# Kernel tuning notes

Hardware: AMD Instinct MI355X
Metric: run time of the kernel (lower is better)

The kernel has to match this reference:

```python
import jax, jax.numpy as jnp
import numpy as np

N_NODES = 100000
N_EDGES = 3200000
IN_DIM, HID_DIM, OUT_DIM = 512, 256, 64


def setup_inputs() -> dict:
    key = jax.random.key(0)
    k1, k2, k3, k4, k5, k6 = jax.random.split(key, 6)
    x = jax.random.normal(k1, (N_NODES, IN_DIM), dtype=jnp.float32)
    src = jax.random.randint(k2, (N_EDGES,), 0, N_NODES, dtype=jnp.int32)
    dst = jax.random.randint(k3, (N_EDGES,), 0, N_NODES, dtype=jnp.int32)
    edge_index = jnp.stack([src, dst])  # [2, E]: row 0 = src (column), row 1 = dst (row)
    edge_weight = jax.random.uniform(k4, (N_EDGES,), dtype=jnp.float32)
    # Xavier-uniform init like nn.init.xavier_uniform_
    lim1 = float(np.sqrt(6.0 / (IN_DIM + HID_DIM)))
    lim2 = float(np.sqrt(6.0 / (HID_DIM + OUT_DIM)))
    W1 = jax.random.uniform(k5, (IN_DIM, HID_DIM), minval=-lim1, maxval=lim1, dtype=jnp.float32)
    W2 = jax.random.uniform(k6, (HID_DIM, OUT_DIM), minval=-lim2, maxval=lim2, dtype=jnp.float32)
    return {"x": x, "edge_index": edge_index, "edge_weight": edge_weight, "W1": W1, "W2": W2}


def _spmm(edge_index, edge_weight, support):
    # out[dst] += w * support[src]  (sparse adjacency @ dense support)
    src, dst = edge_index[0], edge_index[1]
    msgs = support[src] * edge_weight[:, None]  # [E, F]
    return jax.ops.segment_sum(msgs, dst, num_segments=N_NODES)


def reference(x, edge_index, edge_weight, W1, W2):
    # Layer 1: dense GEMM then SpMM, then ReLU (dropout is identity in eval)
    h = _spmm(edge_index, edge_weight, x @ W1)
    h = jax.nn.relu(h)
    # Layer 2
    out = _spmm(edge_index, edge_weight, h @ W2)
    return jax.nn.softmax(out, axis=1)
```

## Files before the change

### kernel.cpp

```cpp
#include <hip/hip_runtime.h>
#include <hip/hip_bf16.h>

typedef __attribute__((ext_vector_type(8))) short bf16x8;
typedef __attribute__((ext_vector_type(4))) float f32x4;
typedef __attribute__((ext_vector_type(4))) _Float16 f16x4;
typedef unsigned short ushort_t;

#define NN   100000
#define NE   3200000
#define IND  512
#define HIDD 256
#define OUTD 64

#define NBKT 98
#define P1E  2048
#define MPAN 782

__device__ __forceinline__ ushort_t f2bf(float a) {
    unsigned u = __float_as_uint(a);
    unsigned r = (u + 0x7FFFu + ((u >> 16) & 1u)) >> 16;
    return (ushort_t)r;
}
__device__ __forceinline__ float bf2f(ushort_t b) {
    return __uint_as_float(((unsigned)b) << 16);
}

union U8 { ushort_t us[8]; unsigned u32[4]; uint4 v; };

#define GLOAD_LDS16(gp, lp) \
    __builtin_amdgcn_global_load_lds( \
        (const __attribute__((address_space(1))) void*)(const void*)(gp), \
        (__attribute__((address_space(3))) void*)(void*)(lp), 16, 0, 0)

__device__ __forceinline__ void split8(float4 v0, float4 v1, bf16x8& aH, bf16x8& aL) {
    float vv[8] = {v0.x, v0.y, v0.z, v0.w, v1.x, v1.y, v1.z, v1.w};
    U8 H, L;
    #pragma unroll
    for (int j = 0; j < 4; ++j) {
        unsigned u0 = __float_as_uint(vv[2 * j]);
        unsigned u1 = __float_as_uint(vv[2 * j + 1]);
        H.u32[j] = __builtin_amdgcn_perm(u1, u0, 0x07060302u);
        float r0 = vv[2 * j]     - __uint_as_float(u0 & 0xFFFF0000u);
        float r1 = vv[2 * j + 1] - __uint_as_float(u1 & 0xFFFF0000u);
        L.u32[j] = __builtin_amdgcn_perm(__float_as_uint(r1),
                                         __float_as_uint(r0), 0x07060302u);
    }
    aH = *(const bf16x8*)&H.v;
    aL = *(const bf16x8*)&L.v;
}

__global__ void splitw_k(const float* __restrict__ in, ushort_t* __restrict__ thi,
                         ushort_t* __restrict__ tlo, int R, int C) {
    int i = blockIdx.x * 256 + threadIdx.x;
    if (i < R * C) {
        int r = i / C, c = i % C;
        float a = in[i];
        ushort_t h = f2bf(a);
        thi[(size_t)c * R + r] = h;
        tlo[(size_t)c * R + r] = f2bf(a - bf2f(h));
    }
}

__global__ __launch_bounds__(256, 3) void gemm1_k(
    const float* __restrict__ A, const ushort_t* __restrict__ BtHi,
    const ushort_t* __restrict__ BtLo, _Float16* __restrict__ C)
{
    const int M = NN, N = HIDD, K = IND;
    __shared__ __align__(16) float    sA [128 * 32];
    __shared__ __align__(16) ushort_t sBh[128 * 32];
    __shared__ __align__(16) ushort_t sBl[128 * 32];

    const int bid   = blockIdx.x;
    const int grp   = bid >> 4;
    const int rr_   = bid & 15;
    const int panel = grp * 8 + (rr_ & 7);
    if (panel >= MPAN) return;
    const int m0 = panel * 128;
    const int n0 = (rr_ >> 3) * 128;

    const int tid  = threadIdx.x;
    const int wave = tid >> 6;
    const int lane = tid & 63;
    const int quad = lane >> 4;
    const int l15  = lane & 15;
    const int wr   = wave >> 1;
    const int wc   = wave & 1;

    const float* aSrc[4];
    float*       aDst[4];
    #pragma unroll
    for (int it = 0; it < 4; ++it) {
        int f = it * 256 + tid;
        int r = f >> 3;
        int bp = (f & 7) ^ ((r & 3) << 1) ^ ((r >> 2) & 1);
        int gr = m0 + r; if (gr >= M) gr = M - 1;
        aSrc[it] = A + (size_t)gr * K + bp * 4;
        aDst[it] = &sA[f * 4];
    }
    const ushort_t* bhSrc[2]; const ushort_t* blSrc[2];
    ushort_t* bhDst[2]; ushort_t* blDst[2];
    #pragma unroll
    for (int it = 0; it < 2; ++it) {
        int f = it * 256 + tid;
        int r = f >> 2;
        int qp = (f & 3) ^ ((r >> 1) & 3);
        bhSrc[it] = BtHi + (size_t)(n0 + r) * K + qp * 8;
        blSrc[it] = BtLo + (size_t)(n0 + r) * K + qp * 8;
        bhDst[it] = &sBh[f * 8];
        blDst[it] = &sBl[f * 8];
    }

    int aOff[4][2];
    #pragma unroll
    for (int ms = 0; ms < 4; ++ms) {
        int rA = wr * 64 + ms * 16 + l15;
        int sw = ((rA & 3) << 1) ^ ((rA >> 2) & 1);
        int cb = quad << 1;
        aOff[ms][0] = rA * 32 + (((cb    ) ^ sw) << 2);
        aOff[ms][1] = rA * 32 + (((cb | 1) ^ sw) << 2);
    }
    int bOff[4];
    #pragma unroll
    for (int ns = 0; ns < 4; ++ns) {
        int rB = wc * 64 + ns * 16 + l15;
        bOff[ns] = rB * 32 + (quad ^ ((rB >> 1) & 3)) * 8;
    }

    f32x4 acc[4][4] = {};

    for (int k0 = 0; k0 < K; k0 += 32) {
        #pragma unroll
        for (int it = 0; it < 4; ++it) GLOAD_LDS16(aSrc[it] + k0, aDst[it]);
        #pragma unroll
        for (int it = 0; it < 2; ++it) {
            GLOAD_LDS16(bhSrc[it] + k0, bhDst[it]);
            GLOAD_LDS16(blSrc[it] + k0, blDst[it]);
        }
        __syncthreads();

        bf16x8 aH[4], aL[4];
        #pragma unroll
        for (int ms = 0; ms < 4; ++ms) {
            float4 v0 = *(const float4*)&sA[aOff[ms][0]];
            float4 v1 = *(const float4*)&sA[aOff[ms][1]];
            split8(v0, v1, aH[ms], aL[ms]);
        }

        #pragma unroll
        for (int ns = 0; ns < 4; ++ns) {
            bf16x8 bH = *(const bf16x8*)&sBh[bOff[ns]];
            bf16x8 bL = *(const bf16x8*)&sBl[bOff[ns]];
            #pragma unroll
            for (int ms = 0; ms < 4; ++ms) {
                acc[ms][ns] = __builtin_amdgcn_mfma_f32_16x16x32_bf16(aH[ms], bH, acc[ms][ns], 0, 0, 0);
                acc[ms][ns] = __builtin_amdgcn_mfma_f32_16x16x32_bf16(aL[ms], bH, acc[ms][ns], 0, 0, 0);
                acc[ms][ns] = __builtin_amdgcn_mfma_f32_16x16x32_bf16(aH[ms], bL, acc[ms][ns], 0, 0, 0);
            }
        }
        __syncthreads();
    }

    #pragma unroll
    for (int ms = 0; ms < 4; ++ms) {
        int row = m0 + wr * 64 + ms * 16 + quad * 4;
        #pragma unroll
        for (int ns = 0; ns < 4; ++ns) {
            int col = n0 + wc * 64 + ns * 16 + l15;
            #pragma unroll
            for (int r = 0; r < 4; ++r)
                if (row + r < M) C[(size_t)(row + r) * N + col] = (_Float16)acc[ms][ns][r];
        }
    }
}

__global__ __launch_bounds__(256) void bhist_k(const int* __restrict__ dst,
                                               int* __restrict__ bucketHist) {
    __shared__ int h[NBKT];
    int t = threadIdx.x;
    if (t < NBKT) h[t] = 0;
    __syncthreads();
    #pragma unroll
    for (int j = 0; j < 4; ++j) {
        int e = blockIdx.x * 1024 + t + j * 256;
        if (e < NE) atomicAdd(&h[dst[e] >> 10], 1);
    }
    __syncthreads();
    if (t < NBKT && h[t]) atomicAdd(&bucketHist[t], h[t]);
}

__global__ __launch_bounds__(128) void bscan_k(const int* __restrict__ bucketHist,
                                               int* __restrict__ bucketStart,
                                               int* __restrict__ bucketCursor) {
    __shared__ int s[128];
    int t = threadIdx.x;
    int v = (t < NBKT) ? bucketHist[t] : 0;
    s[t] = v;
    for (int off = 1; off < 128; off <<= 1) {
        __syncthreads();
        int a = (t >= off) ? s[t - off] : 0;
        __syncthreads();
        s[t] += a;
    }
    __syncthreads();
    if (t < NBKT) { bucketStart[t] = s[t] - v; bucketCursor[t] = s[t] - v; }
    if (t == NBKT - 1) bucketStart[NBKT] = s[t];
}

__global__ __launch_bounds__(256) void phase1_k(
    const int* __restrict__ src, const int* __restrict__ dst,
    const float* __restrict__ w, int* __restrict__ bucketCursor,
    int2* __restrict__ binned)
{
    __shared__ int2 raw[P1E];
    __shared__ int2 ord[P1E];
    __shared__ ushort_t rbkt[P1E], obkt[P1E];
    __shared__ int hist[128], excl[128], cursor[128], gbase[128], stmp[128];

    int t = threadIdx.x;
    if (t < 128) hist[t] = 0;
    __syncthreads();

    int e0 = blockIdx.x * P1E;
    #pragma unroll
    for (int j = 0; j < P1E / 256; ++j) {
        int li = t + j * 256;
        int e = e0 + li;
        if (e < NE) {
            int d = dst[e];
            int b = d >> 10;
            raw[li] = make_int2(src[e] | ((d & 1023) << 17), __float_as_int(w[e]));
            rbkt[li] = (ushort_t)b;
            atomicAdd(&hist[b], 1);
        } else rbkt[li] = 0xFFFFu;
    }
    __syncthreads();
    int v = (t < 128) ? hist[t] : 0;
    if (t < 128) stmp[t] = v;
    for (int off = 1; off < 128; off <<= 1) {
        __syncthreads();
        int a = (t < 128 && t >= off) ? stmp[t - off] : 0;
        __syncthreads();
        if (t < 128) stmp[t] += a;
    }
    __syncthreads();
    if (t < 128) { excl[t] = stmp[t] - v; cursor[t] = stmp[t] - v; }
    if (t < NBKT) gbase[t] = atomicAdd(&bucketCursor[t], hist[t]);
    __syncthreads();
    #pragma unroll
    for (int j = 0; j < P1E / 256; ++j) {
        int li = t + j * 256;
        ushort_t b = rbkt[li];
        if (b != 0xFFFFu) {
            int p = atomicAdd(&cursor[b], 1);
            ord[p] = raw[li];
            obkt[p] = b;
        }
    }
    __syncthreads();
    int tot = excl[NBKT - 1] + hist[NBKT - 1];
    #pragma unroll
    for (int j = 0; j < P1E / 256; ++j) {
        int li = t + j * 256;
        if (li < tot) {
            int b = obkt[li];
            binned[(size_t)gbase[b] + (li - excl[b])] = ord[li];
        }
    }
}

__global__ __launch_bounds__(256) void phase2_k(
    const int* __restrict__ bucketStart, const int2* __restrict__ binned,
    int* __restrict__ rowptr, int2* __restrict__ esw)
{
    __shared__ int cnt[1024], ex[1024], cur[1024], wsum[256];
    int t = threadIdx.x, blk = blockIdx.x;
    int gb = bucketStart[blk], ge = bucketStart[blk + 1];
    #pragma unroll
    for (int j = 0; j < 4; ++j) cnt[t + j * 256] = 0;
    __syncthreads();
    for (int e = gb + t; e < ge; e += 256)
        atomicAdd(&cnt[(binned[e].x >> 17) & 1023], 1);
    __syncthreads();
    int b4 = t * 4;
    int l0 = cnt[b4], l1 = cnt[b4 + 1], l2 = cnt[b4 + 2], l3 = cnt[b4 + 3];
    int ls = l0 + l1 + l2 + l3;
    wsum[t] = ls;
    for (int off = 1; off < 256; off <<= 1) {
        __syncthreads();
        int a = (t >= off) ? wsum[t - off] : 0;
        __syncthreads();
        wsum[t] += a;
    }
    __syncthreads();
    int be = wsum[t] - ls;
    ex[b4] = be;            cur[b4] = be;
    ex[b4 + 1] = be + l0;     cur[b4 + 1] = be + l0;
    ex[b4 + 2] = be + l0 + l1;  cur[b4 + 2] = be + l0 + l1;
    ex[b4 + 3] = be + l0 + l1 + l2; cur[b4 + 3] = be + l0 + l1 + l2;
    __syncthreads();
    int n0 = blk << 10;
    #pragma unroll
    for (int j = 0; j < 4; ++j) {
        int i = b4 + j;
        if (n0 + i < NN) rowptr[n0 + i] = gb + ex[i];
    }
    if (blk == NBKT - 1 && t == 0) rowptr[NN] = NE;
    for (int e = gb + t; e < ge; e += 256) {
        int2 en = binned[e];
        int d = (en.x >> 17) & 1023;
        int p = atomicAdd(&cur[d], 1);
        esw[(size_t)gb + p] = make_int2(en.x & 0x1FFFF, en.y);
    }
}

__global__ __launch_bounds__(256) void spmm_relu_gemm2_k(
    const int* __restrict__ rowptr, const int2* __restrict__ esw,
    const _Float16* __restrict__ X, const ushort_t* __restrict__ BtHi,
    const ushort_t* __restrict__ BtLo, _Float16* __restrict__ S2)
{
    __shared__ __align__(16) float h[16][260];

    const int wave  = threadIdx.x >> 6;
    const int lane  = threadIdx.x & 63;
    const int quad  = lane >> 4;
    const int l15   = lane & 15;
    const int nbase = blockIdx.x * 16;

    const _Float16* Xl = X + lane * 4;
    #pragma unroll
    for (int i = 0; i < 4; ++i) {
        const int ln   = wave * 4 + i;
        const int node = nbase + ln;
        const int beg = rowptr[node], end = rowptr[node + 1];
        f32x4 acc = {0.f, 0.f, 0.f, 0.f};
        #pragma unroll 8
        for (int e = beg; e < end; ++e) {
            int2 sw = esw[e];
            float w = __int_as_float(sw.y);
            f16x4 v = *(const f16x4*)(Xl + (size_t)sw.x * HIDD);
            acc.x += (float)v[0] * w;
            acc.y += (float)v[1] * w;
            acc.z += (float)v[2] * w;
            acc.w += (float)v[3] * w;
        }
        f32x4 r;
        r.x = fmaxf(acc.x, 0.f);
        r.y = fmaxf(acc.y, 0.f);
        r.z = fmaxf(acc.z, 0.f);
        r.w = fmaxf(acc.w, 0.f);
        *(f32x4*)&h[ln][lane * 4] = r;
    }
    __syncthreads();

    f32x4 acc2 = {0.f, 0.f, 0.f, 0.f};
    const ushort_t* bh = BtHi + (size_t)(wave * 16 + l15) * HIDD;
    const ushort_t* bl = BtLo + (size_t)(wave * 16 + l15) * HIDD;
    #pragma unroll
    for (int ks = 0; ks < 8; ++ks) {
        const int ko = ks * 32 + quad * 8;
        const float* ap = &h[l15][ko];
        float4 v0 = *(const float4*)ap;
        float4 v1 = *(const float4*)(ap + 4);
        bf16x8 aH, aL;
        split8(v0, v1, aH, aL);
        bf16x8 bH = *(const bf16x8*)(bh + ko);
        bf16x8 bL = *(const bf16x8*)(bl + ko);
        acc2 = __builtin_amdgcn_mfma_f32_16x16x32_bf16(aH, bH, acc2, 0, 0, 0);
        acc2 = __builtin_amdgcn_mfma_f32_16x16x32_bf16(aL, bH, acc2, 0, 0, 0);
        acc2 = __builtin_amdgcn_mfma_f32_16x16x32_bf16(aH, bL, acc2, 0, 0, 0);
    }
    #pragma unroll
    for (int r = 0; r < 4; ++r) {
        const int node = nbase + quad * 4 + r;
        S2[(size_t)node * OUTD + wave * 16 + l15] = (_Float16)acc2[r];
    }
}

__global__ __launch_bounds__(256) void spmm_softmax_k(
    const int* __restrict__ rowptr, const int2* __restrict__ esw,
    const _Float16* __restrict__ X, float* __restrict__ out)
{
    int node = blockIdx.x * 4 + (threadIdx.x >> 6);
    int lane = threadIdx.x & 63;
    int beg = rowptr[node], end = rowptr[node + 1];
    float acc = 0.f;
    #pragma unroll 4
    for (int e = beg; e < end; ++e) {
        int2 sw = esw[e];
        acc += __int_as_float(sw.y) * (float)X[(size_t)sw.x * OUTD + lane];
    }
    float mx = acc;
    #pragma unroll
    for (int off = 32; off > 0; off >>= 1) mx = fmaxf(mx, __shfl_xor(mx, off));
    float ex = __expf(acc - mx);
    float sm = ex;
    #pragma unroll
    for (int off = 32; off > 0; off >>= 1) sm += __shfl_xor(sm, off);
    out[(size_t)node * OUTD + lane] = ex / sm;
}

extern "C" void kernel_launch(void* const* d_in, const int* in_sizes, int n_in,
                              void* d_out, int out_size, void* d_ws, size_t ws_size,
                              hipStream_t stream) {
    const float* x  = (const float*)d_in[0];
    const int*   ei = (const int*)d_in[1];
    const float* ew = (const float*)d_in[2];
    const float* W1 = (const float*)d_in[3];
    const float* W2 = (const float*)d_in[4];
    float* out = (float*)d_out;
    const int* src = ei;
    const int* dst = ei + NE;

    char* ws = (char*)d_ws;
    size_t o = 0;
    auto take = [&](size_t bytes) -> void* {
        void* p = (void*)(ws + o);
        o += (bytes + 255) & ~(size_t)255;
        return p;
    };
    _Float16* S1      = (_Float16*)take((size_t)NN * HIDD * 2);
    _Float16* S2      = (_Float16*)take((size_t)NN * OUTD * 2);
    int2*     binned  = (int2*    )take((size_t)NE * 8);
    ushort_t* W1tHi   = (ushort_t*)take((size_t)IND * HIDD * 2);
    ushort_t* W1tLo   = (ushort_t*)take((size_t)IND * HIDD * 2);
    ushort_t* W2tHi   = (ushort_t*)take((size_t)HIDD * OUTD * 2);
    ushort_t* W2tLo   = (ushort_t*)take((size_t)HIDD * OUTD * 2);
    int*      rowptr  = (int*     )take((size_t)(NN + 1) * 4);
    int*      bHist   = (int*     )take(NBKT * 4);
    int*      bStart  = (int*     )take((NBKT + 1) * 4);
    int*      bCursor = (int*     )take(NBKT * 4);
    int2*     esw     = (int2*    )take((size_t)NE * 8);
    (void)in_sizes; (void)n_in; (void)out_size; (void)ws_size;

    hipMemsetAsync(bHist, 0, NBKT * 4, stream);
    splitw_k<<<(IND * HIDD + 255) / 256, 256, 0, stream>>>(W1, W1tHi, W1tLo, IND, HIDD);
    splitw_k<<<(HIDD * OUTD + 255) / 256, 256, 0, stream>>>(W2, W2tHi, W2tLo, HIDD, OUTD);

    bhist_k<<<(NE + 1023) / 1024, 256, 0, stream>>>(dst, bHist);
    bscan_k<<<1, 128, 0, stream>>>(bHist, bStart, bCursor);
    phase1_k<<<(NE + P1E - 1) / P1E, 256, 0, stream>>>(src, dst, ew, bCursor, binned);
    phase2_k<<<NBKT, 256, 0, stream>>>(bStart, binned, rowptr, esw);

    const int G1 = ((MPAN + 7) / 8) * 16;
    gemm1_k<<<G1, 256, 0, stream>>>(x, W1tHi, W1tLo, S1);
    spmm_relu_gemm2_k<<<NN / 16, 256, 0, stream>>>(rowptr, esw, S1, W2tHi, W2tLo, S2);
    spmm_softmax_k<<<NN / 4, 256, 0, stream>>>(rowptr, esw, S2, out);
}
```

Before: 889.0 us.

## Process multiple edges per wave in both SpMM gathers with wider loads

In the layer-1 SpMM, each wave now splits into two halves that handle alternate edges with 16-byte f16x8 loads, then combines the partial sums with a cross-half shuffle before ReLU. In the layer-2 SpMM+softmax, each wave splits into four 16-lane groups that each gather a different edge with 8-byte loads, reduces across groups, and computes softmax on four values per lane. The aim is more memory-level parallelism and fewer, wider gather loads per edge for these latency-bound loops. The cost is extra shuffle reductions and tail handling, and fewer lanes are active on the stores.

```diff
diff --git a/kernel.cpp b/kernel.cpp
--- a/kernel.cpp
+++ b/kernel.cpp
@@ -3,7 +3,9 @@
 
 typedef __attribute__((ext_vector_type(8))) short bf16x8;
 typedef __attribute__((ext_vector_type(4))) float f32x4;
+typedef __attribute__((ext_vector_type(8))) float f32x8;
 typedef __attribute__((ext_vector_type(4))) _Float16 f16x4;
+typedef __attribute__((ext_vector_type(8))) _Float16 f16x8;
 typedef unsigned short ushort_t;
 
 #define NN   100000
@@ -324,31 +326,44 @@
     const int lane  = threadIdx.x & 63;
     const int quad  = lane >> 4;
     const int l15   = lane & 15;
+    const int half  = lane >> 5;
+    const int l31   = lane & 31;
     const int nbase = blockIdx.x * 16;
 
-    const _Float16* Xl = X + lane * 4;
+    const _Float16* Xl = X + l31 * 8;
     #pragma unroll
     for (int i = 0; i < 4; ++i) {
         const int ln   = wave * 4 + i;
         const int node = nbase + ln;
         const int beg = rowptr[node], end = rowptr[node + 1];
-        f32x4 acc = {0.f, 0.f, 0.f, 0.f};
-        #pragma unroll 8
-        for (int e = beg; e < end; ++e) {
+        f32x8 acc = {0.f, 0.f, 0.f, 0.f, 0.f, 0.f, 0.f, 0.f};
+        int e = beg;
+        #pragma unroll 4
+        for (; e + 1 < end; e += 2) {
+            int2 sw = esw[e + half];
+            float w = __int_as_float(sw.y);
+            f16x8 v = *(const f16x8*)(Xl + (size_t)sw.x * HIDD);
+            #pragma unroll
+            for (int j = 0; j < 8; ++j) acc[j] += (float)v[j] * w;
+        }
+        if (e < end) {
             int2 sw = esw[e];
-            float w = __int_as_float(sw.y);
-            f16x4 v = *(const f16x4*)(Xl + (size_t)sw.x * HIDD);
-            acc.x += (float)v[0] * w;
-            acc.y += (float)v[1] * w;
-            acc.z += (float)v[2] * w;
-            acc.w += (float)v[3] * w;
-        }
-        f32x4 r;
-        r.x = fmaxf(acc.x, 0.f);
-        r.y = fmaxf(acc.y, 0.f);
-        r.z = fmaxf(acc.z, 0.f);
-        r.w = fmaxf(acc.w, 0.f);
-        *(f32x4*)&h[ln][lane * 4] = r;
+            float w = half ? 0.f : __int_as_float(sw.y);
+            f16x8 v = *(const f16x8*)(Xl + (size_t)sw.x * HIDD);
+            #pragma unroll
+            for (int j = 0; j < 8; ++j) acc[j] += (float)v[j] * w;
+        }
+        #pragma unroll
+        for (int j = 0; j < 8; ++j) acc[j] += __shfl_xor(acc[j], 32);
+        if (half == 0) {
+            float4 r0, r1;
+            r0.x = fmaxf(acc[0], 0.f); r0.y = fmaxf(acc[1], 0.f);
+            r0.z = fmaxf(acc[2], 0.f); r0.w = fmaxf(acc[3], 0.f);
+            r1.x = fmaxf(acc[4], 0.f); r1.y = fmaxf(acc[5], 0.f);
+            r1.z = fmaxf(acc[6], 0.f); r1.w = fmaxf(acc[7], 0.f);
+            *(float4*)&h[ln][l31 * 8]     = r0;
+            *(float4*)&h[ln][l31 * 8 + 4] = r1;
+        }
     }
     __syncthreads();
 
@@ -380,23 +395,53 @@
     const int* __restrict__ rowptr, const int2* __restrict__ esw,
     const _Float16* __restrict__ X, float* __restrict__ out)
 {
-    int node = blockIdx.x * 4 + (threadIdx.x >> 6);
-    int lane = threadIdx.x & 63;
-    int beg = rowptr[node], end = rowptr[node + 1];
-    float acc = 0.f;
+    const int node = blockIdx.x * 4 + (threadIdx.x >> 6);
+    const int lane = threadIdx.x & 63;
+    const int g    = lane >> 4;
+    const int l15  = lane & 15;
+    const int beg = rowptr[node], end = rowptr[node + 1];
+
+    f32x4 acc = {0.f, 0.f, 0.f, 0.f};
+    const _Float16* Xl = X + l15 * 4;
+    int e = beg;
     #pragma unroll 4
-    for (int e = beg; e < end; ++e) {
-        int2 sw = esw[e];
-        acc += __int_as_float(sw.y) * (float)X[(size_t)sw.x * OUTD + lane];
-    }
-    float mx = acc;
-    #pragma unroll
-    for (int off = 32; off > 0; off >>= 1) mx = fmaxf(mx, __shfl_xor(mx, off));
-    float ex = __expf(acc - mx);
-    float sm = ex;
-    #pragma unroll
-    for (int off = 32; off > 0; off >>= 1) sm += __shfl_xor(sm, off);
-    out[(size_t)node * OUTD + lane] = ex / sm;
+    for (; e + 3 < end; e += 4) {
+        int2 sw = esw[e + g];
+        float w = __int_as_float(sw.y);
+        f16x4 v = *(const f16x4*)(Xl + (size_t)sw.x * OUTD);
+        acc.x += (float)v[0] * w;
+        acc.y += (float)v[1] * w;
+        acc.z += (float)v[2] * w;
+        acc.w += (float)v[3] * w;
+    }
+    if (e < end) {
+        int idx = e + g;
+        int2 sw = esw[min(idx, end - 1)];
+        float w = (idx < end) ? __int_as_float(sw.y) : 0.f;
+        f16x4 v = *(const f16x4*)(Xl + (size_t)sw.x * OUTD);
+        acc.x += (float)v[0] * w;
+        acc.y += (float)v[1] * w;
+        acc.z += (float)v[2] * w;
+        acc.w += (float)v[3] * w;
+    }
+    acc.x += __shfl_xor(acc.x, 16); acc.x += __shfl_xor(acc.x, 32);
+    acc.y += __shfl_xor(acc.y, 16); acc.y += __shfl_xor(acc.y, 32);
+    acc.z += __shfl_xor(acc.z, 16); acc.z += __shfl_xor(acc.z, 32);
+    acc.w += __shfl_xor(acc.w, 16); acc.w += __shfl_xor(acc.w, 32);
+
+    float mx = fmaxf(fmaxf(acc.x, acc.y), fmaxf(acc.z, acc.w));
+    #pragma unroll
+    for (int off = 8; off > 0; off >>= 1) mx = fmaxf(mx, __shfl_xor(mx, off));
+    float e0 = __expf(acc.x - mx), e1 = __expf(acc.y - mx);
+    float e2 = __expf(acc.z - mx), e3 = __expf(acc.w - mx);
+    float sm = e0 + e1 + e2 + e3;
+    #pragma unroll
+    for (int off = 8; off > 0; off >>= 1) sm += __shfl_xor(sm, off);
+    if (g == 0) {
+        float inv = 1.f / sm;
+        f32x4 r = {e0 * inv, e1 * inv, e2 * inv, e3 * inv};
+        *(f32x4*)(out + (size_t)node * OUTD + l15 * 4) = r;
+    }
 }
 
 extern "C" void kernel_launch(void* const* d_in, const int* in_sizes, int n_in,
```

Result: faster. 828.0 us (-6.9%).
